# Performance work log

Measured on AMD Instinct MI355X. Metric: run time of the kernel, lower is better.

Reference implementation:

```python
import jax, jax.numpy as jnp
import numpy as np

N_NODES = 50000


def setup_inputs() -> dict:
    key = jax.random.key(0)
    ks = jax.random.split(key, 6)
    F_IN, F_HID, N_EDGES = 128, 512, 800000
    x = jax.random.normal(ks[0], (N_NODES, F_IN), dtype=jnp.float32)
    edge_index = jax.random.randint(ks[1], (2, N_EDGES), 0, N_NODES, dtype=jnp.int64)
    W1 = jax.random.normal(ks[2], (F_IN, F_HID), dtype=jnp.float32) * (1.0 / np.sqrt(F_IN))
    b1 = jnp.zeros((F_HID,), dtype=jnp.float32)
    W2 = jax.random.normal(ks[3], (F_HID, F_IN), dtype=jnp.float32) * (1.0 / np.sqrt(F_HID))
    b2 = jnp.zeros((F_IN,), dtype=jnp.float32)
    eps = jnp.zeros((), dtype=jnp.float32)  # train_eps=True, init 0
    return {"x": x, "edge_index": edge_index, "W1": W1, "b1": b1, "W2": W2, "b2": b2, "eps": eps}


def reference(x, edge_index, W1, b1, W2, b2, eps):
    # GINConv: out = MLP((1+eps)*x + sum_{j in N(i)} x_j)
    src, dst = edge_index[0], edge_index[1]
    agg = jax.ops.segment_sum(x[src], dst, num_segments=N_NODES)  # [N, F]
    h = (1.0 + eps) * x + agg
    h = jax.nn.relu(h @ W1 + b1)
    out = h @ W2 + b2
    return out
```

## Files before the change

### kernel.cpp

```cpp
#include <hip/hip_runtime.h>
#include <hip/hip_bf16.h>

#define N_NODES 50000
#define F_IN    128
#define F_HID   512
#define N_EDGES 800000

#define NBKT 782
#define BKCAP 1280
#define NDMAX 64
#define NZERO 50000

typedef __bf16 bf16x2 __attribute__((ext_vector_type(2)));
typedef __bf16 bf16x4 __attribute__((ext_vector_type(4)));
typedef __bf16 bf16x8 __attribute__((ext_vector_type(8)));
typedef float  f32x4  __attribute__((ext_vector_type(4)));
typedef unsigned short u16x8 __attribute__((ext_vector_type(8)));

#define NB_F 196
#define NB_X 1563
#define NB_W 8
__global__ __launch_bounds__(1024) void fill_prep(const float* __restrict__ x,
                                                  const int* __restrict__ ei,
                                                  const float* __restrict__ W1,
                                                  const float* __restrict__ W2,
                                                  __bf16* __restrict__ xb,
                                                  __bf16* __restrict__ w1f,
                                                  __bf16* __restrict__ w2f,
                                                  int* __restrict__ gcnt,
                                                  int* __restrict__ entries) {
    int b = blockIdx.x, tid = threadIdx.x;
    if (b < NB_F) {
        __shared__ int hist[NBKT], base_[NBKT];
        for (int i = tid; i < NBKT; i += 1024) hist[i] = 0;
        __syncthreads();

        int e0 = (b * 1024 + tid) * 4;
        int bk[4], sl[4], pay[4];
        bool act[4];
        #pragma unroll
        for (int k = 0; k < 4; ++k) {
            int e = e0 + k;
            act[k] = (e < N_EDGES);
            if (act[k]) {
                int src = ei[e];
                int dst = ei[N_EDGES + e];
                bk[k] = dst >> 6;
                pay[k] = ((dst & 63) << 16) | src;
                sl[k] = atomicAdd(&hist[bk[k]], 1);
            }
        }
        __syncthreads();

        for (int i = tid; i < NBKT; i += 1024) {
            int h = hist[i];
            base_[i] = h ? atomicAdd(&gcnt[i * 16], h) : 0;
        }
        __syncthreads();

        #pragma unroll
        for (int k = 0; k < 4; ++k)
            if (act[k]) {
                int p = base_[bk[k]] + sl[k];
                if (p < BKCAP) entries[(size_t)bk[k] * BKCAP + p] = pay[k];
            }
    } else if (b < NB_F + NB_X) {
        int i = (b - NB_F) * 1024 + tid;
        if (i < 1600000) {
            float4 v = ((const float4*)x)[i];
            bf16x4 o = {(__bf16)v.x, (__bf16)v.y, (__bf16)v.z, (__bf16)v.w};
            ((bf16x4*)xb)[i] = o;
        }
    } else if (b < NB_F + NB_X + NB_W) {
        int t = (b - NB_F - NB_X) * 1024 + tid;
        int lane = t & 63, kk = (t >> 6) & 3, nt = (t >> 8) & 7, c = (t >> 11) & 3;
        int q = lane >> 4, l16 = lane & 15;
        bf16x8 o;
        #pragma unroll
        for (int j = 0; j < 8; ++j)
            o[j] = (__bf16)W1[(kk * 32 + q * 8 + j) * F_HID + c * 128 + nt * 16 + l16];
        *(bf16x8*)(w1f + (size_t)t * 8) = o;
    } else {
        int t = (b - NB_F - NB_X - NB_W) * 1024 + tid;
        int lane = t & 63, kk = (t >> 6) & 3, nt = (t >> 8) & 7, c = (t >> 11) & 3;
        int q = lane >> 4, l16 = lane & 15;
        bf16x8 o;
        #pragma unroll
        for (int j = 0; j < 8; ++j)
            o[j] = (__bf16)W2[(c * 128 + kk * 32 + q * 8 + j) * F_IN + nt * 16 + l16];
        *(bf16x8*)(w2f + (size_t)t * 8) = o;
    }
}

__global__ __launch_bounds__(512) void gin_fused(const __bf16* __restrict__ xb,
                                                 const int* __restrict__ gcnt,
                                                 const int* __restrict__ entries,
                                                 const float* __restrict__ eps,
                                                 const __bf16* __restrict__ w1f,
                                                 const __bf16* __restrict__ w2f,
                                                 const float* __restrict__ b1,
                                                 const float* __restrict__ b2,
                                                 float* __restrict__ out) {
    __shared__ union __attribute__((aligned(16))) {
        struct { int degs[64]; unsigned short bin16[64 * NDMAX]; } p0;
        __bf16 Hb[8192];
    } u;
    __shared__ __attribute__((aligned(16))) __bf16 As[8192];

    const int tid = threadIdx.x;
    const int wave = tid >> 6, lane = tid & 63;
    const int q = lane >> 4, l16 = lane & 15;
    const int bkt = blockIdx.x;

    if (tid < 64) u.p0.degs[tid] = 0;
    {
        const int zz = (NZERO << 16) | NZERO;
        int* b32 = (int*)u.p0.bin16;
        #pragma unroll
        for (int k = 0; k < 4; ++k) b32[tid * 4 + k] = zz;
    }
    __syncthreads();

    {
        int cnt = gcnt[bkt * 16];
        cnt = cnt < BKCAP ? cnt : BKCAP;
        const int* eb = entries + (size_t)bkt * BKCAP;
        for (int i = tid; i < cnt; i += 512) {
            int en = eb[i];
            int dl = en >> 16;
            int p = atomicAdd(&u.p0.degs[dl], 1);
            if (p < NDMAX)
                u.p0.bin16[dl * NDMAX + (p & 3) * 16 + (p >> 2)] =
                    (unsigned short)(en & 0xffff);
        }
    }
    __syncthreads();

    const float s = 1.0f + eps[0];
#define ROW(idx) (*(const bf16x8*)(xb + (size_t)(idx) * F_IN + l16 * 8))
    #pragma unroll 2
    for (int t = 0; t < 8; ++t) {
        int n = wave * 8 + t;
        int node = bkt * 64 + n;
        int dg = u.p0.degs[n];
        dg = dg < NDMAX ? dg : NDMAX;
        int myc = (dg + 3 - q) >> 2;
        u16x8 I0 = *(const u16x8*)&u.p0.bin16[n * NDMAX + q * 16];
        u16x8 I1 = *(const u16x8*)&u.p0.bin16[n * NDMAX + q * 16 + 8];

        float acc[8];
        #pragma unroll
        for (int i = 0; i < 8; ++i) acc[i] = 0.0f;
        if (q == 0) {
            bf16x8 self = ROW(node);
            #pragma unroll
            for (int i = 0; i < 8; ++i) acc[i] = (float)self[i] * s;
        }

        bf16x8 ra0 = ROW(I0[0]), ra1 = ROW(I0[1]), ra2 = ROW(I0[2]), ra3 = ROW(I0[3]);
        bf16x8 rb0 = ROW(I0[4]), rb1 = ROW(I0[5]), rb2 = ROW(I0[6]), rb3 = ROW(I0[7]);
        #pragma unroll
        for (int i = 0; i < 8; ++i)
            acc[i] += ((float)ra0[i] + (float)ra1[i]) + ((float)ra2[i] + (float)ra3[i]);
        #pragma unroll
        for (int i = 0; i < 8; ++i)
            acc[i] += ((float)rb0[i] + (float)rb1[i]) + ((float)rb2[i] + (float)rb3[i]);

        if (myc > 8) {
            #pragma unroll
            for (int v = 0; v < 8; ++v)
                if (myc > 8 + v) {
                    bf16x8 r = ROW(I1[v]);
                    #pragma unroll
                    for (int i = 0; i < 8; ++i) acc[i] += (float)r[i];
                }
        }

        #pragma unroll
        for (int i = 0; i < 8; ++i) {
            acc[i] += __shfl_xor(acc[i], 16);
            acc[i] += __shfl_xor(acc[i], 32);
        }
        if (lane < 16) {
            int g = n >> 4, r16 = n & 15;
            bf16x8 o;
            #pragma unroll
            for (int i = 0; i < 8; ++i) o[i] = (__bf16)acc[i];
            int byte = (g * 16 + lane) * 256 + r16 * 16;
            byte ^= (lane & 7) << 4;
            *(bf16x8*)((char*)As + byte) = o;
        }
    }
    __syncthreads();

    const int wr = wave >> 2, wc = wave & 3;

    f32x4 acc_o[2][2];
    #pragma unroll
    for (int ni = 0; ni < 2; ++ni) {
        float bv = b2[wc * 32 + ni * 16 + l16];
        f32x4 b4 = {bv, bv, bv, bv};
        acc_o[0][ni] = b4;
        acc_o[1][ni] = b4;
    }

    for (int c = 0; c < 4; ++c) {
        f32x4 acc_h[2][2];
        #pragma unroll
        for (int ni = 0; ni < 2; ++ni) {
            float bv = b1[c * 128 + wc * 32 + ni * 16 + l16];
            f32x4 b4 = {bv, bv, bv, bv};
            acc_h[0][ni] = b4;
            acc_h[1][ni] = b4;
        }
        #pragma unroll
        for (int kk = 0; kk < 4; ++kk) {
            bf16x8 am[2], bw[2];
            #pragma unroll
            for (int mi = 0; mi < 2; ++mi) {
                int g = wr * 2 + mi;
                int byte = ((g * 4 + kk) * 4 + q) * 256 + l16 * 16;
                byte ^= ((kk * 4 + q) & 7) << 4;
                am[mi] = *(const bf16x8*)((const char*)As + byte);
            }
            #pragma unroll
            for (int ni = 0; ni < 2; ++ni)
                bw[ni] = *(const bf16x8*)(w1f +
                    ((size_t)((c * 8 + wc * 2 + ni) * 4 + kk) << 9) + lane * 8);
            #pragma unroll
            for (int mi = 0; mi < 2; ++mi)
                #pragma unroll
                for (int ni = 0; ni < 2; ++ni)
                    acc_h[mi][ni] = __builtin_amdgcn_mfma_f32_16x16x32_bf16(
                        am[mi], bw[ni], acc_h[mi][ni], 0, 0, 0);
        }
        #pragma unroll
        for (int mi = 0; mi < 2; ++mi) {
            int g = wr * 2 + mi;
            #pragma unroll
            for (int ni = 0; ni < 2; ++ni)
                #pragma unroll
                for (int r = 0; r < 4; ++r)
                    u.Hb[(((g * 4 + wc) * 64 + (ni * 2 + (l16 >> 3)) * 16 + q * 4 + r) << 3)
                         + (l16 & 7)] = (__bf16)fmaxf(acc_h[mi][ni][r], 0.0f);
        }
        __syncthreads();

        #pragma unroll
        for (int kk = 0; kk < 4; ++kk) {
            bf16x8 am[2], bw[2];
            #pragma unroll
            for (int mi = 0; mi < 2; ++mi)
                am[mi] = *(const bf16x8*)&u.Hb[(((wr * 2 + mi) * 4 + kk) * 64 + lane) << 3];
            #pragma unroll
            for (int ni = 0; ni < 2; ++ni)
                bw[ni] = *(const bf16x8*)(w2f +
                    ((size_t)((c * 8 + wc * 2 + ni) * 4 + kk) << 9) + lane * 8);
            #pragma unroll
            for (int mi = 0; mi < 2; ++mi)
                #pragma unroll
                for (int ni = 0; ni < 2; ++ni)
                    acc_o[mi][ni] = __builtin_amdgcn_mfma_f32_16x16x32_bf16(
                        am[mi], bw[ni], acc_o[mi][ni], 0, 0, 0);
        }
        __syncthreads();
    }

    const int m0 = bkt * 64;
    #pragma unroll
    for (int mi = 0; mi < 2; ++mi)
        #pragma unroll
        for (int ni = 0; ni < 2; ++ni)
            #pragma unroll
            for (int r = 0; r < 4; ++r) {
                int m = m0 + wr * 32 + mi * 16 + q * 4 + r;
                if (m < N_NODES)
                    out[(size_t)m * F_IN + wc * 32 + ni * 16 + l16] = acc_o[mi][ni][r];
            }
}

extern "C" void kernel_launch(void* const* d_in, const int* in_sizes, int n_in,
                              void* d_out, int out_size, void* d_ws, size_t ws_size,
                              hipStream_t stream) {
    const float* x   = (const float*)d_in[0];
    const int*   ei  = (const int*)d_in[1];
    const float* W1  = (const float*)d_in[2];
    const float* b1  = (const float*)d_in[3];
    const float* W2  = (const float*)d_in[4];
    const float* b2  = (const float*)d_in[5];
    const float* eps = (const float*)d_in[6];
    float* out = (float*)d_out;

    char* ws = (char*)d_ws;
    __bf16* xb   = (__bf16*)ws;
    __bf16* w1f  = (__bf16*)(ws + 12900000);
    __bf16* w2f  = (__bf16*)(ws + 13100000);
    int*    gcnt = (int*)(ws + 13300000);
    int*    entries = (int*)(ws + 13400000);

    hipMemsetAsync(gcnt, 0, NBKT * 64, stream);
    hipMemsetAsync((char*)ws + (size_t)N_NODES * F_IN * 2, 0, 48 * F_IN * 2, stream);
    fill_prep<<<NB_F + NB_X + 2 * NB_W, 1024, 0, stream>>>(x, ei, W1, W2,
                                                           xb, w1f, w2f, gcnt, entries);
    gin_fused<<<NBKT, 512, 0, stream>>>(xb, gcnt, entries, eps, w1f, w2f, b1, b2, out);
}
```

Measured before the change: 158.7 us.

## Gather neighbor rows via async global_load_lds double-buffered staging

Replaces the per-lane register gather of neighbor rows with a double-buffered pipeline of global_load_lds transfers into per-wave LDS staging buffers. Each step pulls 8 neighbor rows while the previous chunk is summed, and waitcnt instructions control the overlap. The first 32 neighbors go through this pipeline, and higher-degree nodes and the self term are handled afterwards in a separate fix-up pass. It also folds the zero-row memset into the prep kernel, dropping one launch. The cost is an extra 32KB of LDS, which may lower occupancy, plus hand-written wait counts that must stay correct.

```diff
diff --git a/kernel.cpp b/kernel.cpp
--- a/kernel.cpp
+++ b/kernel.cpp
@@ -16,6 +16,9 @@
 typedef __bf16 bf16x8 __attribute__((ext_vector_type(8)));
 typedef float  f32x4  __attribute__((ext_vector_type(4)));
 typedef unsigned short u16x8 __attribute__((ext_vector_type(8)));
+
+typedef __attribute__((address_space(1))) const void glb_cvoid;
+typedef __attribute__((address_space(3))) void lds_void;
 
 #define NB_F 196
 #define NB_X 1563
@@ -80,7 +83,7 @@
         for (int j = 0; j < 8; ++j)
             o[j] = (__bf16)W1[(kk * 32 + q * 8 + j) * F_HID + c * 128 + nt * 16 + l16];
         *(bf16x8*)(w1f + (size_t)t * 8) = o;
-    } else {
+    } else if (b < NB_F + NB_X + 2 * NB_W) {
         int t = (b - NB_F - NB_X - NB_W) * 1024 + tid;
         int lane = t & 63, kk = (t >> 6) & 3, nt = (t >> 8) & 7, c = (t >> 11) & 3;
         int q = lane >> 4, l16 = lane & 15;
@@ -89,6 +92,11 @@
         for (int j = 0; j < 8; ++j)
             o[j] = (__bf16)W2[(c * 128 + kk * 32 + q * 8 + j) * F_IN + nt * 16 + l16];
         *(bf16x8*)(w2f + (size_t)t * 8) = o;
+    } else {
+        if (tid < 16) {
+            uint4 z = {0, 0, 0, 0};
+            ((uint4*)(xb + (size_t)NZERO * F_IN))[tid] = z;
+        }
     }
 }
 
@@ -101,11 +109,12 @@
                                                  const float* __restrict__ b1,
                                                  const float* __restrict__ b2,
                                                  float* __restrict__ out) {
+    __shared__ __attribute__((aligned(16))) __bf16 As[8192];
     __shared__ union __attribute__((aligned(16))) {
         struct { int degs[64]; unsigned short bin16[64 * NDMAX]; } p0;
         __bf16 Hb[8192];
     } u;
-    __shared__ __attribute__((aligned(16))) __bf16 As[8192];
+    __shared__ __attribute__((aligned(16))) __bf16 Stg[8][2][1024];
 
     const int tid = threadIdx.x;
     const int wave = tid >> 6, lane = tid & 63;
@@ -130,65 +139,100 @@
             int dl = en >> 16;
             int p = atomicAdd(&u.p0.degs[dl], 1);
             if (p < NDMAX)
-                u.p0.bin16[dl * NDMAX + (p & 3) * 16 + (p >> 2)] =
-                    (unsigned short)(en & 0xffff);
+                u.p0.bin16[dl * NDMAX + p] = (unsigned short)(en & 0xffff);
         }
     }
     __syncthreads();
 
-    const float s = 1.0f + eps[0];
-#define ROW(idx) (*(const bf16x8*)(xb + (size_t)(idx) * F_IN + l16 * 8))
-    #pragma unroll 2
-    for (int t = 0; t < 8; ++t) {
-        int n = wave * 8 + t;
-        int node = bkt * 64 + n;
-        int dg = u.p0.degs[n];
-        dg = dg < NDMAX ? dg : NDMAX;
-        int myc = (dg + 3 - q) >> 2;
-        u16x8 I0 = *(const u16x8*)&u.p0.bin16[n * NDMAX + q * 16];
-        u16x8 I1 = *(const u16x8*)&u.p0.bin16[n * NDMAX + q * 16 + 8];
-
-        float acc[8];
-        #pragma unroll
-        for (int i = 0; i < 8; ++i) acc[i] = 0.0f;
-        if (q == 0) {
-            bf16x8 self = ROW(node);
-            #pragma unroll
-            for (int i = 0; i < 8; ++i) acc[i] = (float)self[i] * s;
-        }
-
-        bf16x8 ra0 = ROW(I0[0]), ra1 = ROW(I0[1]), ra2 = ROW(I0[2]), ra3 = ROW(I0[3]);
-        bf16x8 rb0 = ROW(I0[4]), rb1 = ROW(I0[5]), rb2 = ROW(I0[6]), rb3 = ROW(I0[7]);
-        #pragma unroll
-        for (int i = 0; i < 8; ++i)
-            acc[i] += ((float)ra0[i] + (float)ra1[i]) + ((float)ra2[i] + (float)ra3[i]);
-        #pragma unroll
-        for (int i = 0; i < 8; ++i)
-            acc[i] += ((float)rb0[i] + (float)rb1[i]) + ((float)rb2[i] + (float)rb3[i]);
-
-        if (myc > 8) {
-            #pragma unroll
-            for (int v = 0; v < 8; ++v)
-                if (myc > 8 + v) {
-                    bf16x8 r = ROW(I1[v]);
+    float s = 1.0f + eps[0];
+    asm volatile("" :: "v"(s));
+
+    __bf16* stA = &Stg[wave][0][0];
+    __bf16* stB = &Stg[wave][1][0];
+
+    float acc[8];
+    #pragma unroll
+    for (int i = 0; i < 8; ++i) acc[i] = 0.0f;
+
+#define ISSUE(k_, buf_) { \
+        int n_ = wave * 8 + ((k_) >> 2); \
+        int sb_ = n_ * NDMAX + ((k_) & 3) * 8; \
+        int i0_ = u.p0.bin16[sb_ + q]; \
+        int i1_ = u.p0.bin16[sb_ + 4 + q]; \
+        __builtin_amdgcn_global_load_lds( \
+            (glb_cvoid*)(xb + (size_t)i0_ * F_IN + l16 * 8), (lds_void*)(buf_), 16, 0, 0); \
+        __builtin_amdgcn_global_load_lds( \
+            (glb_cvoid*)(xb + (size_t)i1_ * F_IN + l16 * 8), (lds_void*)((buf_) + 512), 16, 0, 0); }
+
+#define SUMC(buf_) { \
+        bf16x8 r0_ = *(const bf16x8*)((buf_) + q * 128 + l16 * 8); \
+        bf16x8 r1_ = *(const bf16x8*)((buf_) + 512 + q * 128 + l16 * 8); \
+        _Pragma("unroll") \
+        for (int i = 0; i < 8; ++i) acc[i] += (float)r0_[i] + (float)r1_[i]; }
+
+#define FINISH(k_) { \
+        int n_ = wave * 8 + ((k_) >> 2); \
+        _Pragma("unroll") \
+        for (int i = 0; i < 8; ++i) { acc[i] += __shfl_xor(acc[i], 16); \
+                                      acc[i] += __shfl_xor(acc[i], 32); } \
+        if (lane < 16) { \
+            bf16x8 o_; \
+            _Pragma("unroll") \
+            for (int i = 0; i < 8; ++i) o_[i] = (__bf16)acc[i]; \
+            int byte_ = ((n_ >> 4) * 16 + lane) * 256 + (n_ & 15) * 16; \
+            byte_ ^= (lane & 7) << 4; \
+            *(bf16x8*)((char*)As + byte_) = o_; \
+        } \
+        _Pragma("unroll") \
+        for (int i = 0; i < 8; ++i) acc[i] = 0.0f; }
+
+    ISSUE(0, stA);
+    for (int k = 0; k < 32; k += 2) {
+        asm volatile("s_waitcnt lgkmcnt(0)" ::: "memory");
+        ISSUE(k + 1, stB);
+        asm volatile("s_waitcnt vmcnt(2)" ::: "memory");
+        SUMC(stA);
+        if (k + 2 < 32) {
+            asm volatile("s_waitcnt lgkmcnt(0)" ::: "memory");
+            ISSUE(k + 2, stA);
+            asm volatile("s_waitcnt vmcnt(2)" ::: "memory");
+        } else {
+            asm volatile("s_waitcnt vmcnt(0)" ::: "memory");
+        }
+        SUMC(stB);
+        if (((k + 1) & 3) == 3) FINISH(k + 1);
+    }
+
+    if (lane < 16) {
+        bf16x8 sf[8];
+        #pragma unroll
+        for (int t = 0; t < 8; ++t) {
+            int node = bkt * 64 + wave * 8 + t;
+            sf[t] = *(const bf16x8*)(xb + (size_t)node * F_IN + lane * 8);
+        }
+        #pragma unroll
+        for (int t = 0; t < 8; ++t) {
+            int n = wave * 8 + t;
+            int byte_ = ((n >> 4) * 16 + lane) * 256 + (n & 15) * 16;
+            byte_ ^= (lane & 7) << 4;
+            bf16x8 cur = *(const bf16x8*)((const char*)As + byte_);
+            float v[8];
+            #pragma unroll
+            for (int i = 0; i < 8; ++i) v[i] = (float)cur[i] + s * (float)sf[t][i];
+            int dg = u.p0.degs[n];
+            if (dg > 32) {
+                dg = dg < NDMAX ? dg : NDMAX;
+                for (int r = 32; r < dg; ++r) {
+                    int idx = u.p0.bin16[n * NDMAX + r];
+                    bf16x8 rr = *(const bf16x8*)(xb + (size_t)idx * F_IN + lane * 8);
                     #pragma unroll
-                    for (int i = 0; i < 8; ++i) acc[i] += (float)r[i];
+                    for (int i = 0; i < 8; ++i) v[i] += (float)rr[i];
                 }
-        }
-
-        #pragma unroll
-        for (int i = 0; i < 8; ++i) {
-            acc[i] += __shfl_xor(acc[i], 16);
-            acc[i] += __shfl_xor(acc[i], 32);
-        }
-        if (lane < 16) {
-            int g = n >> 4, r16 = n & 15;
+            }
             bf16x8 o;
             #pragma unroll
-            for (int i = 0; i < 8; ++i) o[i] = (__bf16)acc[i];
-            int byte = (g * 16 + lane) * 256 + r16 * 16;
-            byte ^= (lane & 7) << 4;
-            *(bf16x8*)((char*)As + byte) = o;
+            for (int i = 0; i < 8; ++i) o[i] = (__bf16)v[i];
+            *(bf16x8*)((char*)As + byte_) = o;
         }
     }
     __syncthreads();
@@ -219,9 +263,9 @@
             #pragma unroll
             for (int mi = 0; mi < 2; ++mi) {
                 int g = wr * 2 + mi;
-                int byte = ((g * 4 + kk) * 4 + q) * 256 + l16 * 16;
-                byte ^= ((kk * 4 + q) & 7) << 4;
-                am[mi] = *(const bf16x8*)((const char*)As + byte);
+                int byte_ = ((g * 4 + kk) * 4 + q) * 256 + l16 * 16;
+                byte_ ^= ((kk * 4 + q) & 7) << 4;
+                am[mi] = *(const bf16x8*)((const char*)As + byte_);
             }
             #pragma unroll
             for (int ni = 0; ni < 2; ++ni)
@@ -299,8 +343,7 @@
     int*    entries = (int*)(ws + 13400000);
 
     hipMemsetAsync(gcnt, 0, NBKT * 64, stream);
-    hipMemsetAsync((char*)ws + (size_t)N_NODES * F_IN * 2, 0, 48 * F_IN * 2, stream);
-    fill_prep<<<NB_F + NB_X + 2 * NB_W, 1024, 0, stream>>>(x, ei, W1, W2,
-                                                           xb, w1f, w2f, gcnt, entries);
+    fill_prep<<<NB_F + NB_X + 2 * NB_W + 1, 1024, 0, stream>>>(x, ei, W1, W2,
+                                                               xb, w1f, w2f, gcnt, entries);
     gin_fused<<<NBKT, 512, 0, stream>>>(xb, gcnt, entries, eps, w1f, w2f, b1, b2, out);
 }
```

Result: slower. 172.3 us (+8.6%).
